# Kernel tuning notes

Hardware: AMD Instinct MI355X
Metric: run time of the kernel (lower is better)

The kernel has to match this reference:

```python
import jax, jax.numpy as jnp
import numpy as np
import math

WINDOW = 257
W = (WINDOW - 1) // 2      # 128
Q_CH = WINDOW + 1          # 258 (query chunk size / stride)
K_CH = WINDOW * 2          # 514 (key window size)


def compl_mod(m, n):
    return int(n * math.ceil(m / n) - m)


def setup_inputs() -> dict:
    key = jax.random.key(0)
    k1, k2, k3 = jax.random.split(key, 3)
    b, s, nh, h = 2, 4096, 16, 64
    q = jax.random.normal(k1, (b, s, nh, h), jnp.float32)
    k = jax.random.normal(k2, (b, s, nh, h), jnp.float32)
    v = jax.random.normal(k3, (b, s, nh, h), jnp.float32)
    return {"q": q, "k": k, "v": v}


def reference(q, k, v):
    b, s, nh, h = q.shape
    q = q * h ** (-0.5)
    q_pad = compl_mod(s, Q_CH)
    k_pad = compl_mod(s + 2 * W - K_CH, Q_CH)
    c = (s + q_pad) // Q_CH  # number of chunks

    # pad along sequence dim (q right-padded; k/v haloed by w on both sides)
    qp = jnp.pad(q, ((0, 0), (0, q_pad), (0, 0), (0, 0)))
    kp = jnp.pad(k, ((0, 0), (W, W + k_pad), (0, 0), (0, 0)))
    vp = jnp.pad(v, ((0, 0), (W, W + k_pad), (0, 0), (0, 0)))

    # unfold: q non-overlapping chunks, k/v overlapping windows (size K_CH, stride Q_CH)
    qw = qp.reshape(b, c, Q_CH, nh, h)                              # [b,c,q,nh,h]
    idx = (jnp.arange(c) * Q_CH)[:, None] + jnp.arange(K_CH)[None]  # [c,K_CH]
    kw = kp[:, idx]                                                 # [b,c,k,nh,h]
    vw = vp[:, idx]

    A = jnp.einsum('bcqnh,bcknh->bncqk', qw, kw)  # [b,nh,c,Q_CH,K_CH]

    # banded mask: valid iff i <= j <= i + 2w (True = masked)
    i = jnp.arange(Q_CH)[:, None]
    j = jnp.arange(K_CH)[None, :]
    base = ~((j >= i) & (j <= i + 2 * W))
    mask_left = base.at[:, :W].set(True)                    # first chunk: no left halo
    mask_right = base.at[:, K_CH - (W + k_pad):].set(True)  # last chunk: no right halo/pad
    if c > 1:
        mask = jnp.concatenate(
            [mask_left[None], jnp.broadcast_to(base, (c - 2, Q_CH, K_CH)), mask_right[None]], axis=0)
    else:
        mask = (mask_left | mask_right)[None]

    mask_value = -jnp.finfo(A.dtype).max
    A = jnp.where(mask[None, None], mask_value, A)
    A = jax.nn.softmax(A, axis=-1)  # dropout omitted (eval mode)

    z = jnp.einsum('bncqk,bcknh->bncqh', A, vw)       # [b,nh,c,Q_CH,h]
    z = z.reshape(b, nh, c * Q_CH, h)[:, :, :s]       # trim q padding
    return jnp.transpose(z, (0, 2, 1, 3))             # [b,s,nh,h]
```

## Files before the change

kernel.cpp:

```cpp
#include <hip/hip_runtime.h>

typedef _Float16 h16;
typedef __attribute__((ext_vector_type(2))) _Float16 f16x2;
typedef __attribute__((ext_vector_type(4))) _Float16 f16x4;
typedef __attribute__((ext_vector_type(2))) __fp16   fp16x2n;
typedef __attribute__((ext_vector_type(8))) _Float16 f16x8;
typedef __attribute__((ext_vector_type(4))) float f32x4;
typedef __attribute__((ext_vector_type(4))) int   i32x4;

#define S_LEN 4096
#define NHEAD 16
#define HDIM  64
#define WIN   128
#define TQ    256
#define NQT   (S_LEN / TQ)
#define NCH   16
#define KSTR  72
#define VSTR2 40
#define QSCALE 0.18033688011112042f

static __device__ __forceinline__ f16x2 pk(float a, float b) {
    fp16x2n r = __builtin_amdgcn_cvt_pkrtz(a, b);
    return __builtin_bit_cast(f16x2, r);
}

static __device__ __forceinline__ f16x8 cvt8(float4 a, float4 b) {
    f16x2 p0 = pk(a.x, a.y), p1 = pk(a.z, a.w);
    f16x2 p2 = pk(b.x, b.y), p3 = pk(b.z, b.w);
    f16x8 r;
    r[0]=p0[0]; r[1]=p0[1]; r[2]=p1[0]; r[3]=p1[1];
    r[4]=p2[0]; r[5]=p2[1]; r[6]=p3[0]; r[7]=p3[1];
    return r;
}

__global__ __launch_bounds__(512, 4)
void wattn(const float* __restrict__ Qg, const float* __restrict__ Kg,
           const float* __restrict__ Vg, float* __restrict__ Og)
{
    __shared__ h16 Kbuf[3][32 * KSTR];
    __shared__ h16 Vbuf[3][64 * VSTR2];

    const int tid  = threadIdx.x;
    const int wid  = tid >> 6;
    const int lane = tid & 63;
    const int l15  = lane & 15;
    const int quad = lane >> 4;

    int lin = blockIdx.x + NQT * (blockIdx.y + NHEAD * blockIdx.z);
    int nwg = NQT * NHEAD * gridDim.z;
    int swz = ((nwg & 7) == 0) ? ((lin & 7) * (nwg >> 3) + (lin >> 3)) : lin;
    const int bx   = swz & (NQT - 1);
    const int head = (swz / NQT) & (NHEAD - 1);
    const int b    = swz / (NQT * NHEAD);

    const int q0    = bx * TQ;
    const int kbase = q0 - WIN;
    const int rowstride = NHEAD * HDIM;

    const float* KB = Kg + ((long)b * S_LEN * NHEAD + head) * HDIM;
    const float* VB = Vg + ((long)b * S_LEN * NHEAD + head) * HDIM;

    const int srow = tid >> 4;
    const int ish  = tid & 15;
    const int sh0  = ish * 4;
    const int vkey = ((srow + (((ish >> 2) & 3) << 3)) & 31) ^ ((ish & 3) << 3);

    float4 kreg, vreg;
    #define SLOAD(i) do {                                                    \
        int kg_ = kbase + (i)*32 + srow;                                     \
        kg_ = kg_ < 0 ? 0 : (kg_ > S_LEN-1 ? S_LEN-1 : kg_);                 \
        const float* kp_ = KB + (long)kg_ * rowstride + sh0;                 \
        const float* vp_ = VB + (long)kg_ * rowstride + sh0;                 \
        kreg = *(const float4*)kp_;                                          \
        vreg = *(const float4*)vp_;                                          \
    } while (0)
    #define SWRITE(i) do {                                                   \
        int bi_ = (i) % 3;                                                   \
        f16x2 ka_ = pk(kreg.x, kreg.y), kb_ = pk(kreg.z, kreg.w);            \
        f16x4 kv_; kv_[0]=ka_[0]; kv_[1]=ka_[1]; kv_[2]=kb_[0]; kv_[3]=kb_[1];\
        *(f16x4*)&Kbuf[bi_][srow * KSTR + sh0] = kv_;                        \
        Vbuf[bi_][(sh0+0) * VSTR2 + vkey] = (h16)vreg.x;                     \
        Vbuf[bi_][(sh0+1) * VSTR2 + vkey] = (h16)vreg.y;                     \
        Vbuf[bi_][(sh0+2) * VSTR2 + vkey] = (h16)vreg.z;                     \
        Vbuf[bi_][(sh0+3) * VSTR2 + vkey] = (h16)vreg.w;                     \
    } while (0)

    SLOAD(0);

    f16x8 aQ[2][2];
    #pragma unroll
    for (int t2 = 0; t2 < 2; ++t2) {
        const int qrow = q0 + wid*32 + t2*16 + l15;
        const float* qp = Qg + ((long)(b * S_LEN + qrow) * NHEAD + head) * HDIM;
        float4 x0 = *(const float4*)(qp + quad*8);
        float4 x1 = *(const float4*)(qp + quad*8 + 4);
        float4 x2 = *(const float4*)(qp + 32 + quad*8);
        float4 x3 = *(const float4*)(qp + 32 + quad*8 + 4);
        x0.x*=QSCALE; x0.y*=QSCALE; x0.z*=QSCALE; x0.w*=QSCALE;
        x1.x*=QSCALE; x1.y*=QSCALE; x1.z*=QSCALE; x1.w*=QSCALE;
        x2.x*=QSCALE; x2.y*=QSCALE; x2.z*=QSCALE; x2.w*=QSCALE;
        x3.x*=QSCALE; x3.y*=QSCALE; x3.z*=QSCALE; x3.w*=QSCALE;
        aQ[t2][0] = cvt8(x0, x1);
        aQ[t2][1] = cvt8(x2, x3);
    }

    SWRITE(0);
    SLOAD(1);
    __syncthreads();

    int lo[2]; unsigned span[2];
    #pragma unroll
    for (int t2 = 0; t2 < 2; ++t2) {
        const int qg = q0 + wid*32 + t2*16 + l15;
        lo[t2] = (qg - WIN < 0) ? 0 : qg - WIN;
        const int hi = (qg + WIN > S_LEN-1) ? S_LEN-1 : qg + WIN;
        span[t2] = (unsigned)(hi - lo[t2]);
    }

    float l_lane[2] = {0.f, 0.f};
    f32x4 Oacc[2][4];
    #pragma unroll
    for (int t2 = 0; t2 < 2; ++t2)
        #pragma unroll
        for (int t = 0; t < 4; ++t) Oacc[t2][t] = (f32x4){0.f,0.f,0.f,0.f};

    const int pxr = (l15 & 12) << 1;
    const int xl = (quad == 1 || quad == 2) ? (lane ^ 48) : lane;

    for (int i = 0; i < NCH; ++i) {
        if (i + 1 < NCH) SWRITE(i + 1);
        if (i + 2 < NCH) SLOAD(i + 2);

        if ((unsigned)(i - wid) < 9u) {
            const h16* Kb = Kbuf[i % 3];
            const h16* Vb = Vbuf[i % 3];

            f32x4 s0[2], s1[2];
            {
                f16x8 bK00 = *(const f16x8*)&Kb[ l15      * KSTR + quad*8];
                f16x8 bK01 = *(const f16x8*)&Kb[ l15      * KSTR + 32 + quad*8];
                #pragma unroll
                for (int t2 = 0; t2 < 2; ++t2) {
                    f32x4 z = (f32x4){0.f,0.f,0.f,0.f};
                    z = __builtin_amdgcn_mfma_f32_16x16x32_f16(bK00, aQ[t2][0], z, 0, 0, 0);
                    z = __builtin_amdgcn_mfma_f32_16x16x32_f16(bK01, aQ[t2][1], z, 0, 0, 0);
                    s0[t2] = z;
                }
                f16x8 bK10 = *(const f16x8*)&Kb[(16+l15)  * KSTR + quad*8];
                f16x8 bK11 = *(const f16x8*)&Kb[(16+l15)  * KSTR + 32 + quad*8];
                #pragma unroll
                for (int t2 = 0; t2 < 2; ++t2) {
                    f32x4 z = (f32x4){0.f,0.f,0.f,0.f};
                    z = __builtin_amdgcn_mfma_f32_16x16x32_f16(bK10, aQ[t2][0], z, 0, 0, 0);
                    z = __builtin_amdgcn_mfma_f32_16x16x32_f16(bK11, aQ[t2][1], z, 0, 0, 0);
                    s1[t2] = z;
                }
            }

            f16x8 aP[2];
            const int colb = kbase + i*32 + quad*4;
            #pragma unroll
            for (int t2 = 0; t2 < 2; ++t2) {
                float pl[4], ph[4];
                #pragma unroll
                for (int r = 0; r < 4; ++r) {
                    int c_ = colb + r;
                    float v0 = ((unsigned)(c_      - lo[t2]) <= span[t2]) ? s0[t2][r] : -1e30f;
                    float v1 = ((unsigned)(c_ + 16 - lo[t2]) <= span[t2]) ? s1[t2][r] : -1e30f;
                    pl[r] = exp2f(v0);
                    ph[r] = exp2f(v1);
                }
                l_lane[t2] += ((pl[0]+pl[1]) + (pl[2]+pl[3]))
                            + ((ph[0]+ph[1]) + (ph[2]+ph[3]));

                int u0 = __builtin_bit_cast(int, pk(pl[0], pl[1]));
                int u1 = __builtin_bit_cast(int, pk(pl[2], pl[3]));
                int u2 = __builtin_bit_cast(int, pk(ph[0], ph[1]));
                int u3 = __builtin_bit_cast(int, pk(ph[2], ph[3]));
                {
                    const bool q0b = (quad & 1);
                    int s0w = q0b ? u0 : u2;
                    int s1w = q0b ? u1 : u3;
                    int r0 = __builtin_amdgcn_ds_swizzle(s0w, 0x401F);
                    int r1 = __builtin_amdgcn_ds_swizzle(s1w, 0x401F);
                    if (q0b) { u0 = r0; u1 = r1; } else { u2 = r0; u3 = r1; }
                }
                u0 = __shfl(u0, xl);  u1 = __shfl(u1, xl);
                u2 = __shfl(u2, xl);  u3 = __shfl(u3, xl);
                i32x4 uu; uu[0]=u0; uu[1]=u1; uu[2]=u2; uu[3]=u3;
                aP[t2] = __builtin_bit_cast(f16x8, uu);
            }

            #pragma unroll
            for (int t = 0; t < 4; ++t) {
                f16x8 bV = *(const f16x8*)&Vb[(t*16 + l15) * VSTR2 +
                                              (((quad*8 + (t << 3)) & 31) ^ pxr)];
                Oacc[0][t] = __builtin_amdgcn_mfma_f32_16x16x32_f16(aP[0], bV, Oacc[0][t], 0, 0, 0);
                Oacc[1][t] = __builtin_amdgcn_mfma_f32_16x16x32_f16(aP[1], bV, Oacc[1][t], 0, 0, 0);
            }
        }

        __syncthreads();
    }
    #undef SLOAD
    #undef SWRITE

    #pragma unroll
    for (int t2 = 0; t2 < 2; ++t2) {
        float l = l_lane[t2];
        l += __shfl_xor(l, 16);
        l += __shfl_xor(l, 32);
        const float inv = 1.0f / l;

        float* op = Og + ((long)(b * S_LEN + q0 + wid*32 + t2*16) * NHEAD + head) * HDIM;
        #pragma unroll
        for (int r = 0; r < 4; ++r) {
            float invr = __shfl(inv, quad*4 + r);
            #pragma unroll
            for (int t = 0; t < 4; ++t) {
                op[(quad*4 + r) * rowstride + t*16 + l15] = Oacc[t2][t][r] * invr;
            }
        }
    }
}

extern "C" void kernel_launch(void* const* d_in, const int* in_sizes, int n_in,
                              void* d_out, int out_size, void* d_ws, size_t ws_size,
                              hipStream_t stream) {
    const float* q = (const float*)d_in[0];
    const float* k = (const float*)d_in[1];
    const float* v = (const float*)d_in[2];
    float* out = (float*)d_out;
    const int batch = in_sizes[0] / (S_LEN * NHEAD * HDIM);
    dim3 grid(NQT, NHEAD, batch);
    wattn<<<grid, 512, 0, stream>>>(q, k, v, out);
}
```

Baseline: 148.7 us.

## Preload all K/V halo chunks into LDS and drop per-chunk barriers

Replaces the triple-buffered streamed K/V pipeline with a single upfront load of all 16 key/value chunks into LDS, followed by one barrier. Each wave then loops over only its 9 relevant chunks without synchronization. This removes per-iteration __syncthreads and the predicated skip, but the LDS footprint grows to about 155 KB. Launch bounds drop to one block per CU, so occupancy falls and load latency is no longer overlapped with compute.

After: 151.7 us. 2.0% more time.

```diff
diff --git a/kernel.cpp b/kernel.cpp
--- a/kernel.cpp
+++ b/kernel.cpp
@@ -33,12 +33,12 @@
     return r;
 }
 
-__global__ __launch_bounds__(512, 4)
+__global__ __launch_bounds__(512, 1)
 void wattn(const float* __restrict__ Qg, const float* __restrict__ Kg,
            const float* __restrict__ Vg, float* __restrict__ Og)
 {
-    __shared__ h16 Kbuf[3][32 * KSTR];
-    __shared__ h16 Vbuf[3][64 * VSTR2];
+    __shared__ h16 Khalo[NCH][32 * KSTR];
+    __shared__ h16 Vhalo[NCH][64 * VSTR2];
 
     const int tid  = threadIdx.x;
     const int wid  = tid >> 6;
@@ -65,27 +65,30 @@
     const int sh0  = ish * 4;
     const int vkey = ((srow + (((ish >> 2) & 3) << 3)) & 31) ^ ((ish & 3) << 3);
 
-    float4 kreg, vreg;
-    #define SLOAD(i) do {                                                    \
-        int kg_ = kbase + (i)*32 + srow;                                     \
-        kg_ = kg_ < 0 ? 0 : (kg_ > S_LEN-1 ? S_LEN-1 : kg_);                 \
-        const float* kp_ = KB + (long)kg_ * rowstride + sh0;                 \
-        const float* vp_ = VB + (long)kg_ * rowstride + sh0;                 \
-        kreg = *(const float4*)kp_;                                          \
-        vreg = *(const float4*)vp_;                                          \
+    float4 ka, va, kb, vb;
+    #define CLMP(x) ((x) < 0 ? 0 : ((x) > S_LEN-1 ? S_LEN-1 : (x)))
+    #define SLOADA(i) do {                                                   \
+        int kg_ = CLMP(kbase + (i)*32 + srow);                               \
+        ka = *(const float4*)(KB + (long)kg_ * rowstride + sh0);             \
+        va = *(const float4*)(VB + (long)kg_ * rowstride + sh0);             \
     } while (0)
-    #define SWRITE(i) do {                                                   \
-        int bi_ = (i) % 3;                                                   \
-        f16x2 ka_ = pk(kreg.x, kreg.y), kb_ = pk(kreg.z, kreg.w);            \
-        f16x4 kv_; kv_[0]=ka_[0]; kv_[1]=ka_[1]; kv_[2]=kb_[0]; kv_[3]=kb_[1];\
-        *(f16x4*)&Kbuf[bi_][srow * KSTR + sh0] = kv_;                        \
-        Vbuf[bi_][(sh0+0) * VSTR2 + vkey] = (h16)vreg.x;                     \
-        Vbuf[bi_][(sh0+1) * VSTR2 + vkey] = (h16)vreg.y;                     \
-        Vbuf[bi_][(sh0+2) * VSTR2 + vkey] = (h16)vreg.z;                     \
-        Vbuf[bi_][(sh0+3) * VSTR2 + vkey] = (h16)vreg.w;                     \
+    #define SLOADB(i) do {                                                   \
+        int kg_ = CLMP(kbase + (i)*32 + srow);                               \
+        kb = *(const float4*)(KB + (long)kg_ * rowstride + sh0);             \
+        vb = *(const float4*)(VB + (long)kg_ * rowstride + sh0);             \
     } while (0)
-
-    SLOAD(0);
+    #define SWR(i, kr_, vr_) do {                                           \
+        f16x2 p0_ = pk(kr_.x, kr_.y), p1_ = pk(kr_.z, kr_.w);               \
+        f16x4 kv_; kv_[0]=p0_[0]; kv_[1]=p0_[1]; kv_[2]=p1_[0]; kv_[3]=p1_[1];\
+        *(f16x4*)&Khalo[i][srow * KSTR + sh0] = kv_;                        \
+        Vhalo[i][(sh0+0) * VSTR2 + vkey] = (h16)vr_.x;                      \
+        Vhalo[i][(sh0+1) * VSTR2 + vkey] = (h16)vr_.y;                      \
+        Vhalo[i][(sh0+2) * VSTR2 + vkey] = (h16)vr_.z;                      \
+        Vhalo[i][(sh0+3) * VSTR2 + vkey] = (h16)vr_.w;                      \
+    } while (0)
+
+    SLOADA(0);
+    SLOADB(1);
 
     f16x8 aQ[2][2];
     #pragma unroll
@@ -104,9 +107,18 @@
         aQ[t2][1] = cvt8(x2, x3);
     }
 
-    SWRITE(0);
-    SLOAD(1);
+    #pragma unroll
+    for (int p = 0; p < NCH; p += 2) {
+        SWR(p, ka, va);
+        if (p + 2 < NCH) SLOADA(p + 2);
+        SWR(p + 1, kb, vb);
+        if (p + 3 < NCH) SLOADB(p + 3);
+    }
     __syncthreads();
+    #undef SLOADA
+    #undef SLOADB
+    #undef SWR
+    #undef CLMP
 
     int lo[2]; unsigned span[2];
     #pragma unroll
@@ -127,83 +139,76 @@
     const int pxr = (l15 & 12) << 1;
     const int xl = (quad == 1 || quad == 2) ? (lane ^ 48) : lane;
 
-    for (int i = 0; i < NCH; ++i) {
-        if (i + 1 < NCH) SWRITE(i + 1);
-        if (i + 2 < NCH) SLOAD(i + 2);
-
-        if ((unsigned)(i - wid) < 9u) {
-            const h16* Kb = Kbuf[i % 3];
-            const h16* Vb = Vbuf[i % 3];
-
-            f32x4 s0[2], s1[2];
+    #pragma unroll 3
+    for (int ii = 0; ii < 9; ++ii) {
+        const int i = wid + ii;
+        const h16* Kb = Khalo[i];
+        const h16* Vb = Vhalo[i];
+
+        f32x4 s0[2], s1[2];
+        {
+            f16x8 bK00 = *(const f16x8*)&Kb[ l15      * KSTR + quad*8];
+            f16x8 bK01 = *(const f16x8*)&Kb[ l15      * KSTR + 32 + quad*8];
+            #pragma unroll
+            for (int t2 = 0; t2 < 2; ++t2) {
+                f32x4 z = (f32x4){0.f,0.f,0.f,0.f};
+                z = __builtin_amdgcn_mfma_f32_16x16x32_f16(bK00, aQ[t2][0], z, 0, 0, 0);
+                z = __builtin_amdgcn_mfma_f32_16x16x32_f16(bK01, aQ[t2][1], z, 0, 0, 0);
+                s0[t2] = z;
+            }
+            f16x8 bK10 = *(const f16x8*)&Kb[(16+l15)  * KSTR + quad*8];
+            f16x8 bK11 = *(const f16x8*)&Kb[(16+l15)  * KSTR + 32 + quad*8];
+            #pragma unroll
+            for (int t2 = 0; t2 < 2; ++t2) {
+                f32x4 z = (f32x4){0.f,0.f,0.f,0.f};
+                z = __builtin_amdgcn_mfma_f32_16x16x32_f16(bK10, aQ[t2][0], z, 0, 0, 0);
+                z = __builtin_amdgcn_mfma_f32_16x16x32_f16(bK11, aQ[t2][1], z, 0, 0, 0);
+                s1[t2] = z;
+            }
+        }
+
+        f16x8 aP[2];
+        const int colb = kbase + i*32 + quad*4;
+        #pragma unroll
+        for (int t2 = 0; t2 < 2; ++t2) {
+            float pl[4], ph[4];
+            #pragma unroll
+            for (int r = 0; r < 4; ++r) {
+                int c_ = colb + r;
+                float v0 = ((unsigned)(c_      - lo[t2]) <= span[t2]) ? s0[t2][r] : -1e30f;
+                float v1 = ((unsigned)(c_ + 16 - lo[t2]) <= span[t2]) ? s1[t2][r] : -1e30f;
+                pl[r] = exp2f(v0);
+                ph[r] = exp2f(v1);
+            }
+            l_lane[t2] += ((pl[0]+pl[1]) + (pl[2]+pl[3]))
+                        + ((ph[0]+ph[1]) + (ph[2]+ph[3]));
+
+            int u0 = __builtin_bit_cast(int, pk(pl[0], pl[1]));
+            int u1 = __builtin_bit_cast(int, pk(pl[2], pl[3]));
+            int u2 = __builtin_bit_cast(int, pk(ph[0], ph[1]));
+            int u3 = __builtin_bit_cast(int, pk(ph[2], ph[3]));
             {
-                f16x8 bK00 = *(const f16x8*)&Kb[ l15      * KSTR + quad*8];
-                f16x8 bK01 = *(const f16x8*)&Kb[ l15      * KSTR + 32 + quad*8];
-                #pragma unroll
-                for (int t2 = 0; t2 < 2; ++t2) {
-                    f32x4 z = (f32x4){0.f,0.f,0.f,0.f};
-                    z = __builtin_amdgcn_mfma_f32_16x16x32_f16(bK00, aQ[t2][0], z, 0, 0, 0);
-                    z = __builtin_amdgcn_mfma_f32_16x16x32_f16(bK01, aQ[t2][1], z, 0, 0, 0);
-                    s0[t2] = z;
-                }
-                f16x8 bK10 = *(const f16x8*)&Kb[(16+l15)  * KSTR + quad*8];
-                f16x8 bK11 = *(const f16x8*)&Kb[(16+l15)  * KSTR + 32 + quad*8];
-                #pragma unroll
-                for (int t2 = 0; t2 < 2; ++t2) {
-                    f32x4 z = (f32x4){0.f,0.f,0.f,0.f};
-                    z = __builtin_amdgcn_mfma_f32_16x16x32_f16(bK10, aQ[t2][0], z, 0, 0, 0);
-                    z = __builtin_amdgcn_mfma_f32_16x16x32_f16(bK11, aQ[t2][1], z, 0, 0, 0);
-                    s1[t2] = z;
-                }
-            }
-
-            f16x8 aP[2];
-            const int colb = kbase + i*32 + quad*4;
-            #pragma unroll
-            for (int t2 = 0; t2 < 2; ++t2) {
-                float pl[4], ph[4];
-                #pragma unroll
-                for (int r = 0; r < 4; ++r) {
-                    int c_ = colb + r;
-                    float v0 = ((unsigned)(c_      - lo[t2]) <= span[t2]) ? s0[t2][r] : -1e30f;
-                    float v1 = ((unsigned)(c_ + 16 - lo[t2]) <= span[t2]) ? s1[t2][r] : -1e30f;
-                    pl[r] = exp2f(v0);
-                    ph[r] = exp2f(v1);
-                }
-                l_lane[t2] += ((pl[0]+pl[1]) + (pl[2]+pl[3]))
-                            + ((ph[0]+ph[1]) + (ph[2]+ph[3]));
-
-                int u0 = __builtin_bit_cast(int, pk(pl[0], pl[1]));
-                int u1 = __builtin_bit_cast(int, pk(pl[2], pl[3]));
-                int u2 = __builtin_bit_cast(int, pk(ph[0], ph[1]));
-                int u3 = __builtin_bit_cast(int, pk(ph[2], ph[3]));
-                {
-                    const bool q0b = (quad & 1);
-                    int s0w = q0b ? u0 : u2;
-                    int s1w = q0b ? u1 : u3;
-                    int r0 = __builtin_amdgcn_ds_swizzle(s0w, 0x401F);
-                    int r1 = __builtin_amdgcn_ds_swizzle(s1w, 0x401F);
-                    if (q0b) { u0 = r0; u1 = r1; } else { u2 = r0; u3 = r1; }
-                }
-                u0 = __shfl(u0, xl);  u1 = __shfl(u1, xl);
-                u2 = __shfl(u2, xl);  u3 = __shfl(u3, xl);
-                i32x4 uu; uu[0]=u0; uu[1]=u1; uu[2]=u2; uu[3]=u3;
-                aP[t2] = __builtin_bit_cast(f16x8, uu);
-            }
-
-            #pragma unroll
-            for (int t = 0; t < 4; ++t) {
-                f16x8 bV = *(const f16x8*)&Vb[(t*16 + l15) * VSTR2 +
-                                              (((quad*8 + (t << 3)) & 31) ^ pxr)];
-                Oacc[0][t] = __builtin_amdgcn_mfma_f32_16x16x32_f16(aP[0], bV, Oacc[0][t], 0, 0, 0);
-                Oacc[1][t] = __builtin_amdgcn_mfma_f32_16x16x32_f16(aP[1], bV, Oacc[1][t], 0, 0, 0);
-            }
-        }
-
-        __syncthreads();
-    }
-    #undef SLOAD
-    #undef SWRITE
+                const bool q0b = (quad & 1);
+                int s0w = q0b ? u0 : u2;
+                int s1w = q0b ? u1 : u3;
+                int r0 = __builtin_amdgcn_ds_swizzle(s0w, 0x401F);
+                int r1 = __builtin_amdgcn_ds_swizzle(s1w, 0x401F);
+                if (q0b) { u0 = r0; u1 = r1; } else { u2 = r0; u3 = r1; }
+            }
+            u0 = __shfl(u0, xl);  u1 = __shfl(u1, xl);
+            u2 = __shfl(u2, xl);  u3 = __shfl(u3, xl);
+            i32x4 uu; uu[0]=u0; uu[1]=u1; uu[2]=u2; uu[3]=u3;
+            aP[t2] = __builtin_bit_cast(f16x8, uu);
+        }
+
+        #pragma unroll
+        for (int t = 0; t < 4; ++t) {
+            f16x8 bV = *(const f16x8*)&Vb[(t*16 + l15) * VSTR2 +
+                                          (((quad*8 + (t << 3)) & 31) ^ pxr)];
+            Oacc[0][t] = __builtin_amdgcn_mfma_f32_16x16x32_f16(aP[0], bV, Oacc[0][t], 0, 0, 0);
+            Oacc[1][t] = __builtin_amdgcn_mfma_f32_16x16x32_f16(aP[1], bV, Oacc[1][t], 0, 0, 0);
+        }
+    }
 
     #pragma unroll
     for (int t2 = 0; t2 < 2; ++t2) {
```
